# Performance work log

Measured on AMD Instinct MI355X. Metric: run time of the kernel, lower is better.

The kernel has to match this reference:

```python
import jax, jax.numpy as jnp
import numpy as np

MASK_FILL = jnp.float32(-2**32 + 1)

def dice(x, alpha):
    # x: (S, B, F); batch-dim (dim=0) mean/std, unbiased std like torch.std
    avg = x.mean(axis=0)
    std = jnp.std(x, axis=0, ddof=1)
    p = jax.nn.sigmoid((x - avg) / std)
    return x * p + alpha * x * (1.0 - p)

def setup_inputs() -> dict:
    key = jax.random.key(0)
    ks = jax.random.split(key, 12)
    S, B, D = 200, 1024, 128          # seq_len, batch, 2H
    F = 4 * D                          # num_features = 512
    L1, L2 = 80, 40
    inp = {
        "query": jax.random.normal(ks[0], (B, D), jnp.float32),
        "facts": jax.random.normal(ks[1], (S, B, D), jnp.float32),
        "mask": jax.random.randint(ks[2], (S, B), 0, 2).astype(bool),
        "W1": jax.random.normal(ks[3], (F, L1), jnp.float32) / np.sqrt(F),
        "b1": jnp.zeros((L1,), jnp.float32),
        "a1": jnp.zeros((1,), jnp.float32),
        "W2": jax.random.normal(ks[4], (L1, L2), jnp.float32) / np.sqrt(L1),
        "b2": jnp.zeros((L2,), jnp.float32),
        "a2": jnp.zeros((1,), jnp.float32),
        "W3": jax.random.normal(ks[5], (L2, 1), jnp.float32) / np.sqrt(L2),
        "b3": jnp.zeros((1,), jnp.float32),
    }
    return inp

def reference(query, facts, mask, W1, b1, a1, W2, b2, a2, W3, b3):
    S, B, D = facts.shape
    # faithful to torch: tile along feature dim then reshape (permutes elements)
    q2 = jnp.tile(query, (1, S)).reshape(S, B, D)
    x = jnp.concatenate([q2, facts, q2 * facts, q2 - facts], axis=-1)  # (S,B,4D)
    h = dice(jnp.einsum('sbf,fl->sbl', x, W1) + b1, a1)
    h = dice(jnp.einsum('sbf,fl->sbl', h, W2) + b2, a2)
    logits = (jnp.einsum('sbf,fl->sbl', h, W3) + b3).squeeze(-1)  # (S,B)
    masked = jnp.where(mask, logits, MASK_FILL)
    normalized = jax.nn.softmax(masked, axis=0)
    return normalized[..., None] * facts  # (S,B,D)
```

## Files before the change

### kernel.cpp

```cpp
#include <hip/hip_runtime.h>
#include <hip/hip_bf16.h>
#include <math.h>

#define SS 200
#define BB 1024
#define DD 128
#define FF 512
#define LL1 80
#define LL2 40
#define PP (SS*BB)
#define MASK_FILL_F (-4294967295.0f)

typedef short bf16x8 __attribute__((ext_vector_type(8)));
typedef float f32x4  __attribute__((ext_vector_type(4)));

static __device__ __forceinline__ unsigned short f2bf(float x) {
    __hip_bfloat16 h = __float2bfloat16(x);
    return *reinterpret_cast<unsigned short*>(&h);
}
static __device__ __forceinline__ float bf2f(unsigned short u) {
    __hip_bfloat16 h = *reinterpret_cast<__hip_bfloat16*>(&u);
    return __bfloat162float(h);
}
static __device__ __forceinline__ void split8(const float* x, bf16x8& ah, bf16x8& al) {
#pragma unroll
    for (int j = 0; j < 8; ++j) {
        unsigned u = __float_as_uint(x[j]);
        ah[j] = (short)(u >> 16);
        float hi = __uint_as_float(u & 0xffff0000u);
        al[j] = (short)f2bf(x[j] - hi);
    }
}

__global__ void k_prep_all(const float* __restrict__ W1, const float* __restrict__ W2,
                           const unsigned char* __restrict__ mask,
                           unsigned short* __restrict__ bfr1,
                           unsigned short* __restrict__ bfr2, int* __restrict__ flag) {
    const int blk = blockIdx.x;
    if (blk == 35) {
        if (threadIdx.x == 0) {
            int f = 0;
            for (int i = 0; i < 256; ++i)
                if ((i & 3) && mask[i]) f = 1;
            *flag = f;
        }
        return;
    }
    if (blk < 30) {
        int t = blk * 256 + threadIdx.x;
        if (t >= 120 * 64) return;
        int lane = t & 63;
        int fid  = t >> 6;
        int nt   = fid % 5;
        int hl   = (fid / 5) % 2;
        int step = (fid / 10) % 6;
        int h    = fid / 60;
        int ktL  = step / 3;
        int seg  = step - 3 * ktL;
        int kt   = h * 2 + ktL;
        int n     = nt * 16 + (lane & 15);
        int kbase = kt * 32 + (lane >> 4) * 8;
        unsigned short* o = bfr1 + (size_t)t * 8;
#pragma unroll
        for (int j = 0; j < 8; ++j) {
            int k = kbase + j;
            float w;
            if (seg == 0)      w = W1[k * LL1 + n] + W1[(384 + k) * LL1 + n];
            else if (seg == 1) w = W1[(128 + k) * LL1 + n] - W1[(384 + k) * LL1 + n];
            else               w = W1[(256 + k) * LL1 + n];
            unsigned short hb = f2bf(w);
            o[j] = (hl == 0) ? hb : f2bf(w - bf2f(hb));
        }
    } else {
        int t = (blk - 30) * 256 + threadIdx.x;
        if (t >= 18 * 64) return;
        int lane = t & 63;
        int fid  = t >> 6;
        int hl   = fid & 1;
        int nt   = (fid >> 1) % 3;
        int kt   = fid / 6;
        int n  = nt * 16 + (lane & 15);
        int kb = kt * 32 + (lane >> 4) * 8;
        unsigned short* o = bfr2 + (size_t)t * 8;
#pragma unroll
        for (int j = 0; j < 8; ++j) {
            int k = kb + j;
            float w = (k < LL1 && n < LL2) ? W2[k * LL2 + n] : 0.f;
            unsigned short hb = f2bf(w);
            o[j] = (hl == 0) ? hb : f2bf(w - bf2f(hb));
        }
    }
}

__global__ __launch_bounds__(256, 2) void k1_mfma(
    const float* __restrict__ query, const float* __restrict__ facts,
    const unsigned short* __restrict__ bfr, const float* __restrict__ b1,
    float* __restrict__ z1) {
    const int tid  = threadIdx.x;
    const int lane = tid & 63;
    const int m    = lane & 15;
    const int quad = lane >> 4;
    const int pw   = blockIdx.x * 128 + (tid >> 6) * 32;

    __shared__ unsigned short lbuf[30720];

    f32x4 acc[2][5];
#pragma unroll
    for (int t = 0; t < 2; ++t)
#pragma unroll
        for (int nt = 0; nt < 5; ++nt) acc[t][nt] = (f32x4){0.f, 0.f, 0.f, 0.f};

    int pr[2], qr[2];
#pragma unroll
    for (int t = 0; t < 2; ++t) {
        pr[t] = pw + t * 16 + m;
        qr[t] = pr[t] / SS;
    }

    float q8[2][2][8], f8[2][2][8];

#pragma unroll 1
    for (int h = 0; h < 2; ++h) {
#pragma unroll
        for (int ktL = 0; ktL < 2; ++ktL) {
            const int dbase = (h * 2 + ktL) * 32 + quad * 8;
#pragma unroll
            for (int t = 0; t < 2; ++t) {
                *(float4*)&q8[ktL][t][0] = *(const float4*)(query + (size_t)qr[t] * DD + dbase);
                *(float4*)&q8[ktL][t][4] = *(const float4*)(query + (size_t)qr[t] * DD + dbase + 4);
                *(float4*)&f8[ktL][t][0] = *(const float4*)(facts + (size_t)pr[t] * DD + dbase);
                *(float4*)&f8[ktL][t][4] = *(const float4*)(facts + (size_t)pr[t] * DD + dbase + 4);
            }
        }
        if (h) __syncthreads();
        {
            const int4* src = (const int4*)bfr + h * 3840 + tid;
#pragma unroll
            for (int it = 0; it < 15; ++it) {
                int4 v = src[it * 256];
                *(int4*)((char*)lbuf + it * 4096 + tid * 16) = v;
            }
        }
        __syncthreads();

#pragma unroll
        for (int ktL = 0; ktL < 2; ++ktL) {
#pragma unroll
            for (int seg = 0; seg < 3; ++seg) {
                const int step = ktL * 3 + seg;
                bf16x8 Bh[5], Bl[5];
#pragma unroll
                for (int nt = 0; nt < 5; ++nt) {
                    Bh[nt] = *(const bf16x8*)&lbuf[((step * 2 + 0) * 5 + nt) * 512 + lane * 8];
                    Bl[nt] = *(const bf16x8*)&lbuf[((step * 2 + 1) * 5 + nt) * 512 + lane * 8];
                }
#pragma unroll
                for (int t = 0; t < 2; ++t) {
                    float x8[8];
#pragma unroll
                    for (int j = 0; j < 8; ++j)
                        x8[j] = (seg == 0) ? q8[ktL][t][j]
                              : (seg == 1 ? f8[ktL][t][j]
                                          : q8[ktL][t][j] * f8[ktL][t][j]);
                    bf16x8 ah, al;
                    split8(x8, ah, al);
#pragma unroll
                    for (int nt = 0; nt < 5; ++nt) {
                        acc[t][nt] = __builtin_amdgcn_mfma_f32_16x16x32_bf16(ah, Bh[nt], acc[t][nt], 0, 0, 0);
                        acc[t][nt] = __builtin_amdgcn_mfma_f32_16x16x32_bf16(al, Bh[nt], acc[t][nt], 0, 0, 0);
                        acc[t][nt] = __builtin_amdgcn_mfma_f32_16x16x32_bf16(ah, Bl[nt], acc[t][nt], 0, 0, 0);
                    }
                }
            }
        }
    }
#pragma unroll
    for (int t = 0; t < 2; ++t)
#pragma unroll
        for (int nt = 0; nt < 5; ++nt) {
            int n = nt * 16 + m;
            float bias = b1[n];
#pragma unroll
            for (int r = 0; r < 4; ++r)
                z1[(size_t)(pw + t * 16 + quad * 4 + r) * LL1 + n] = acc[t][nt][r] + bias;
        }
}

__global__ __launch_bounds__(256) void k_msd(
    const float* __restrict__ z, float* __restrict__ mean, float* __restrict__ istd) {
    const int col = blockIdx.x * 256 + threadIdx.x;
    const float* p = z + col;
    float s = 0.f, q = 0.f;
#pragma unroll 10
    for (int i = 0; i < SS; ++i) {
        float v = p[(size_t)i * (BB * LL1)];
        s += v;
        q = fmaf(v, v, q);
    }
    float mn = s * (1.f / SS);
    float var = (q - (float)SS * mn * mn) * (1.f / (SS - 1));
    mean[col] = mn;
    istd[col] = rsqrtf(var);
}

__global__ __launch_bounds__(256, 4) void k2_mfma(
    const float* __restrict__ z1, const float* __restrict__ mean1,
    const float* __restrict__ istd1, const float* __restrict__ a1,
    const unsigned short* __restrict__ bfr2, const float* __restrict__ b2,
    float* __restrict__ z2T) {
    const int tid  = threadIdx.x;
    const int lane = tid & 63;
    const int m    = lane & 15;
    const int quad = lane >> 4;
    const int pw   = blockIdx.x * 128 + (tid >> 6) * 32;
    const float alpha = *a1;

    __shared__ unsigned short lb2[9216];
    for (int i = tid; i < 1152; i += 256)
        ((int4*)lb2)[i] = ((const int4*)bfr2)[i];
    __syncthreads();

    f32x4 acc[2][3];
#pragma unroll
    for (int t = 0; t < 2; ++t)
#pragma unroll
        for (int nt = 0; nt < 3; ++nt) acc[t][nt] = (f32x4){0.f, 0.f, 0.f, 0.f};

    float b2v[3];
#pragma unroll
    for (int nt = 0; nt < 3; ++nt) {
        int n = nt * 16 + m;
        b2v[nt] = (n < LL2) ? b2[n] : 0.f;
    }

#pragma unroll
    for (int kt = 0; kt < 3; ++kt) {
        bf16x8 Bh[3], Bl[3];
#pragma unroll
        for (int nt = 0; nt < 3; ++nt) {
            Bh[nt] = *(const bf16x8*)&lb2[((kt * 3 + nt) * 2 + 0) * 512 + lane * 8];
            Bl[nt] = *(const bf16x8*)&lb2[((kt * 3 + nt) * 2 + 1) * 512 + lane * 8];
        }
        const int kb = kt * 32 + quad * 8;
        const bool live = (kt < 2 || quad < 2);
#pragma unroll
        for (int t = 0; t < 2; ++t) {
            const int p = pw + t * 16 + m;
            const int b = p & (BB - 1);
            float x8[8];
            if (live) {
                const float* zr = z1    + (size_t)p * LL1 + kb;
                const float* mu = mean1 + (size_t)b * LL1 + kb;
                const float* is = istd1 + (size_t)b * LL1 + kb;
                float vv[8], mv[8], iv[8];
                *(float4*)&vv[0] = *(const float4*)zr;
                *(float4*)&vv[4] = *(const float4*)(zr + 4);
                *(float4*)&mv[0] = *(const float4*)mu;
                *(float4*)&mv[4] = *(const float4*)(mu + 4);
                *(float4*)&iv[0] = *(const float4*)is;
                *(float4*)&iv[4] = *(const float4*)(is + 4);
#pragma unroll
                for (int j = 0; j < 8; ++j) {
                    float pp = 1.f / (1.f + expf(-(vv[j] - mv[j]) * iv[j]));
                    x8[j] = vv[j] * (alpha + (1.f - alpha) * pp);
                }
            } else {
#pragma unroll
                for (int j = 0; j < 8; ++j) x8[j] = 0.f;
            }
            bf16x8 ah, al;
            split8(x8, ah, al);
#pragma unroll
            for (int nt = 0; nt < 3; ++nt) {
                acc[t][nt] = __builtin_amdgcn_mfma_f32_16x16x32_bf16(ah, Bh[nt], acc[t][nt], 0, 0, 0);
                acc[t][nt] = __builtin_amdgcn_mfma_f32_16x16x32_bf16(al, Bh[nt], acc[t][nt], 0, 0, 0);
                acc[t][nt] = __builtin_amdgcn_mfma_f32_16x16x32_bf16(ah, Bl[nt], acc[t][nt], 0, 0, 0);
            }
        }
    }
#pragma unroll
    for (int t = 0; t < 2; ++t)
#pragma unroll
        for (int r = 0; r < 4; ++r) {
            const int prow = pw + t * 16 + quad * 4 + r;
            const int br = prow & (BB - 1);
            const int sr = prow >> 10;
            float* o = z2T + (size_t)br * (SS * LL2) + (size_t)sr * LL2;
#pragma unroll
            for (int nt = 0; nt < 3; ++nt) {
                int n = nt * 16 + m;
                if (n < LL2) o[n] = acc[t][nt][r] + b2v[nt];
            }
        }
}

__global__ __launch_bounds__(256) void k3_fused(
    const float* __restrict__ z2T, const float* __restrict__ a2,
    const float* __restrict__ W3, const float* __restrict__ b3,
    const void* __restrict__ mask, const int* __restrict__ flag,
    float* __restrict__ wbufT) {
    const int b   = blockIdx.x;
    const int tid = threadIdx.x;
    __shared__ float lds[SS * 41];
    __shared__ float psum[6 * LL2], pssq[6 * LL2];
    __shared__ float smean[LL2], sistd[LL2], sw3[LL2];
    __shared__ float red[4];

    const float4* src = (const float4*)(z2T + (size_t)b * (SS * LL2));
    for (int i = tid; i < (SS * LL2) / 4; i += 256) {
        float4 v = src[i];
        int s = i / 10;
        int o = (i - s * 10) * 4;
        float* d = &lds[s * 41 + o];
        d[0] = v.x; d[1] = v.y; d[2] = v.z; d[3] = v.w;
    }
    __syncthreads();
    if (tid < 240) {
        int l = tid % LL2, c = tid / LL2;
        int s0 = c * 34, s1 = (c == 5) ? SS : s0 + 34;
        float sum = 0.f, ssq = 0.f;
        for (int s = s0; s < s1; ++s) {
            float v = lds[s * 41 + l];
            sum += v;
            ssq = fmaf(v, v, ssq);
        }
        psum[c * LL2 + l] = sum;
        pssq[c * LL2 + l] = ssq;
    }
    __syncthreads();
    if (tid < LL2) {
        float sum = 0.f, ssq = 0.f;
#pragma unroll
        for (int c = 0; c < 6; ++c) {
            sum += psum[c * LL2 + tid];
            ssq += pssq[c * LL2 + tid];
        }
        float mean = sum * (1.f / SS);
        float var  = (ssq - (float)SS * mean * mean) * (1.f / (SS - 1));
        smean[tid] = mean;
        sistd[tid] = rsqrtf(var);
        sw3[tid]   = W3[tid];
    }
    __syncthreads();
    const float alpha = *a2;
    const int boolLayout = *flag;

    float logit = -3.0e38f;
    if (tid < SS) {
        float dot = b3[0];
#pragma unroll
        for (int k = 0; k < LL2; ++k) {
            float v  = lds[tid * 41 + k];
            float pp = 1.f / (1.f + expf(-(v - smean[k]) * sistd[k]));
            float h  = v * (pp + alpha * (1.f - pp));
            dot = fmaf(h, sw3[k], dot);
        }
        int mi = tid * BB + b;
        bool mk = boolLayout ? (((const unsigned char*)mask)[mi] != 0)
                             : (((const int*)mask)[mi] != 0);
        logit = mk ? dot : MASK_FILL_F;
    }
    float v = logit;
#pragma unroll
    for (int off = 1; off < 64; off <<= 1) v = fmaxf(v, __shfl_xor(v, off, 64));
    if ((tid & 63) == 0) red[tid >> 6] = v;
    __syncthreads();
    float smax = fmaxf(fmaxf(red[0], red[1]), fmaxf(red[2], red[3]));
    __syncthreads();
    float e = (tid < SS) ? expf(logit - smax) : 0.f;
    v = e;
#pragma unroll
    for (int off = 1; off < 64; off <<= 1) v += __shfl_xor(v, off, 64);
    if ((tid & 63) == 0) red[tid >> 6] = v;
    __syncthreads();
    float inv = 1.f / (red[0] + red[1] + red[2] + red[3]);
    if (tid < SS) wbufT[(size_t)b * SS + tid] = e * inv;
}

__global__ __launch_bounds__(256) void k4_scale(
    const float* __restrict__ wbufT, const float* __restrict__ facts,
    float* __restrict__ out) {
    int i = blockIdx.x * 256 + threadIdx.x;
    int p = i >> 5;
    float w = wbufT[(size_t)(p & (BB - 1)) * SS + (p >> 10)];
    float4 f = ((const float4*)facts)[i];
    float4 o;
    o.x = f.x * w; o.y = f.y * w; o.z = f.z * w; o.w = f.w * w;
    ((float4*)out)[i] = o;
}

extern "C" void kernel_launch(void* const* d_in, const int* in_sizes, int n_in,
                              void* d_out, int out_size, void* d_ws, size_t ws_size,
                              hipStream_t stream) {
    const float* query = (const float*)d_in[0];
    const float* facts = (const float*)d_in[1];
    const void*  mask  = d_in[2];
    const float* W1 = (const float*)d_in[3];
    const float* b1 = (const float*)d_in[4];
    const float* a1 = (const float*)d_in[5];
    const float* W2 = (const float*)d_in[6];
    const float* b2 = (const float*)d_in[7];
    const float* a2 = (const float*)d_in[8];
    const float* W3 = (const float*)d_in[9];
    const float* b3 = (const float*)d_in[10];
    float* out = (float*)d_out;

    float* z1  = out;
    float* z2T = out + (size_t)PP * LL1;
    float* mean1 = out + 24576000;
    float* istd1 = out + 24657920;
    unsigned short* bfr1 = (unsigned short*)(out + 24739840);
    unsigned short* bfr2 = (unsigned short*)(out + 24801280);
    float* wbufT = (float*)d_ws;
    int*   flag  = (int*)((char*)d_ws + 900 * 1024);

    k_prep_all<<<36, 256, 0, stream>>>(W1, W2, (const unsigned char*)mask, bfr1, bfr2, flag);
    k1_mfma<<<PP / 128, 256, 0, stream>>>(query, facts, bfr1, b1, z1);
    k_msd<<<(BB * LL1) / 256, 256, 0, stream>>>(z1, mean1, istd1);
    k2_mfma<<<PP / 128, 256, 0, stream>>>(z1, mean1, istd1, a1, bfr2, b2, z2T);
    k3_fused<<<BB, 256, 0, stream>>>(z2T, a2, W3, b3, mask, flag, wbufT);
    k4_scale<<<(PP * DD) / (256 * 4), 256, 0, stream>>>(wbufT, facts, out);
}
```

Baseline: 311.6 us.

## Fuse MLP layers, batch-norm stats, softmax and scaling into one per-batch kernel

```diff
diff --git a/kernel.cpp b/kernel.cpp
--- a/kernel.cpp
+++ b/kernel.cpp
@@ -10,6 +10,7 @@
 #define LL2 40
 #define PP (SS*BB)
 #define MASK_FILL_F (-4294967295.0f)
+#define NTILE 13
 
 typedef short bf16x8 __attribute__((ext_vector_type(8)));
 typedef float f32x4  __attribute__((ext_vector_type(4)));
@@ -92,177 +93,174 @@
     }
 }
 
-__global__ __launch_bounds__(256, 2) void k1_mfma(
+__global__ __launch_bounds__(256, 2) void k_fused(
     const float* __restrict__ query, const float* __restrict__ facts,
-    const unsigned short* __restrict__ bfr, const float* __restrict__ b1,
-    float* __restrict__ z1) {
+    const unsigned short* __restrict__ bfr1, const unsigned short* __restrict__ bfr2,
+    const float* __restrict__ b1, const float* __restrict__ a1,
+    const float* __restrict__ b2, const float* __restrict__ a2,
+    const float* __restrict__ W3, const float* __restrict__ b3,
+    const void* __restrict__ mask, const int* __restrict__ flag,
+    float* __restrict__ out) {
     const int tid  = threadIdx.x;
+    const int w    = tid >> 6;
     const int lane = tid & 63;
     const int m    = lane & 15;
     const int quad = lane >> 4;
-    const int pw   = blockIdx.x * 128 + (tid >> 6) * 32;
-
-    __shared__ unsigned short lbuf[30720];
-
-    f32x4 acc[2][5];
-#pragma unroll
-    for (int t = 0; t < 2; ++t)
+    const int b    = blockIdx.x;
+
+    __shared__ __align__(16) float z1f[NTILE * 16 * 81 + 16];
+    __shared__ float psum[240], pssq[240];
+    __shared__ float smean[LL1], sistd[LL1];
+    __shared__ float sw3[LL2];
+    __shared__ float red[4];
+    __shared__ float wgt[SS];
+
+    int tile[4], pr[4], qr[4];
+    bool tl[4];
+#pragma unroll
+    for (int t = 0; t < 4; ++t) {
+        tile[t] = t * 4 + w;
+        tl[t]   = (tile[t] < NTILE);
+        int s = tile[t] * 16 + m;
+        if (s > SS - 1) s = SS - 1;
+        pr[t] = s * BB + b;
+        qr[t] = pr[t] / SS;
+    }
+
+    f32x4 acc[4][5];
+#pragma unroll
+    for (int t = 0; t < 4; ++t)
 #pragma unroll
         for (int nt = 0; nt < 5; ++nt) acc[t][nt] = (f32x4){0.f, 0.f, 0.f, 0.f};
-
-    int pr[2], qr[2];
-#pragma unroll
-    for (int t = 0; t < 2; ++t) {
-        pr[t] = pw + t * 16 + m;
-        qr[t] = pr[t] / SS;
-    }
-
-    float q8[2][2][8], f8[2][2][8];
 
 #pragma unroll 1
     for (int h = 0; h < 2; ++h) {
+        if (h) __syncthreads();
+        {
+            const int4* src = (const int4*)bfr1 + h * 3840 + tid;
+            int4* dst = (int4*)z1f;
+#pragma unroll
+            for (int it = 0; it < 15; ++it)
+                dst[it * 256 + tid] = src[it * 256];
+        }
+        __syncthreads();
+        const unsigned short* lbuf = (const unsigned short*)z1f;
 #pragma unroll
         for (int ktL = 0; ktL < 2; ++ktL) {
             const int dbase = (h * 2 + ktL) * 32 + quad * 8;
 #pragma unroll
-            for (int t = 0; t < 2; ++t) {
-                *(float4*)&q8[ktL][t][0] = *(const float4*)(query + (size_t)qr[t] * DD + dbase);
-                *(float4*)&q8[ktL][t][4] = *(const float4*)(query + (size_t)qr[t] * DD + dbase + 4);
-                *(float4*)&f8[ktL][t][0] = *(const float4*)(facts + (size_t)pr[t] * DD + dbase);
-                *(float4*)&f8[ktL][t][4] = *(const float4*)(facts + (size_t)pr[t] * DD + dbase + 4);
-            }
-        }
-        if (h) __syncthreads();
-        {
-            const int4* src = (const int4*)bfr + h * 3840 + tid;
-#pragma unroll
-            for (int it = 0; it < 15; ++it) {
-                int4 v = src[it * 256];
-                *(int4*)((char*)lbuf + it * 4096 + tid * 16) = v;
-            }
-        }
-        __syncthreads();
-
-#pragma unroll
-        for (int ktL = 0; ktL < 2; ++ktL) {
-#pragma unroll
-            for (int seg = 0; seg < 3; ++seg) {
-                const int step = ktL * 3 + seg;
-                bf16x8 Bh[5], Bl[5];
-#pragma unroll
-                for (int nt = 0; nt < 5; ++nt) {
-                    Bh[nt] = *(const bf16x8*)&lbuf[((step * 2 + 0) * 5 + nt) * 512 + lane * 8];
-                    Bl[nt] = *(const bf16x8*)&lbuf[((step * 2 + 1) * 5 + nt) * 512 + lane * 8];
+            for (int tp = 0; tp < 2; ++tp) {
+                float q8[2][8], f8[2][8];
+#pragma unroll
+                for (int u = 0; u < 2; ++u) {
+                    const int t = tp * 2 + u;
+                    const float* qp = query + (size_t)qr[t] * DD + dbase;
+                    const float* fp = facts + (size_t)pr[t] * DD + dbase;
+                    *(float4*)&q8[u][0] = *(const float4*)qp;
+                    *(float4*)&q8[u][4] = *(const float4*)(qp + 4);
+                    *(float4*)&f8[u][0] = *(const float4*)fp;
+                    *(float4*)&f8[u][4] = *(const float4*)(fp + 4);
                 }
 #pragma unroll
-                for (int t = 0; t < 2; ++t) {
-                    float x8[8];
-#pragma unroll
-                    for (int j = 0; j < 8; ++j)
-                        x8[j] = (seg == 0) ? q8[ktL][t][j]
-                              : (seg == 1 ? f8[ktL][t][j]
-                                          : q8[ktL][t][j] * f8[ktL][t][j]);
-                    bf16x8 ah, al;
-                    split8(x8, ah, al);
+                for (int seg = 0; seg < 3; ++seg) {
+                    const int step = ktL * 3 + seg;
+                    bf16x8 Bh[5], Bl[5];
 #pragma unroll
                     for (int nt = 0; nt < 5; ++nt) {
-                        acc[t][nt] = __builtin_amdgcn_mfma_f32_16x16x32_bf16(ah, Bh[nt], acc[t][nt], 0, 0, 0);
-                        acc[t][nt] = __builtin_amdgcn_mfma_f32_16x16x32_bf16(al, Bh[nt], acc[t][nt], 0, 0, 0);
-                        acc[t][nt] = __builtin_amdgcn_mfma_f32_16x16x32_bf16(ah, Bl[nt], acc[t][nt], 0, 0, 0);
+                        Bh[nt] = *(const bf16x8*)&lbuf[((step * 2 + 0) * 5 + nt) * 512 + lane * 8];
+                        Bl[nt] = *(const bf16x8*)&lbuf[((step * 2 + 1) * 5 + nt) * 512 + lane * 8];
+                    }
+#pragma unroll
+                    for (int u = 0; u < 2; ++u) {
+                        const int t = tp * 2 + u;
+                        if (!tl[t]) continue;
+                        float x8[8];
+#pragma unroll
+                        for (int j = 0; j < 8; ++j)
+                            x8[j] = (seg == 0) ? q8[u][j]
+                                  : (seg == 1 ? f8[u][j] : q8[u][j] * f8[u][j]);
+                        bf16x8 ah, al;
+                        split8(x8, ah, al);
+#pragma unroll
+                        for (int nt = 0; nt < 5; ++nt) {
+                            acc[t][nt] = __builtin_amdgcn_mfma_f32_16x16x32_bf16(ah, Bh[nt], acc[t][nt], 0, 0, 0);
+                            acc[t][nt] = __builtin_amdgcn_mfma_f32_16x16x32_bf16(al, Bh[nt], acc[t][nt], 0, 0, 0);
+                            acc[t][nt] = __builtin_amdgcn_mfma_f32_16x16x32_bf16(ah, Bl[nt], acc[t][nt], 0, 0, 0);
+                        }
                     }
                 }
             }
         }
     }
-#pragma unroll
-    for (int t = 0; t < 2; ++t)
-#pragma unroll
-        for (int nt = 0; nt < 5; ++nt) {
-            int n = nt * 16 + m;
-            float bias = b1[n];
-#pragma unroll
-            for (int r = 0; r < 4; ++r)
-                z1[(size_t)(pw + t * 16 + quad * 4 + r) * LL1 + n] = acc[t][nt][r] + bias;
-        }
-}
-
-__global__ __launch_bounds__(256) void k_msd(
-    const float* __restrict__ z, float* __restrict__ mean, float* __restrict__ istd) {
-    const int col = blockIdx.x * 256 + threadIdx.x;
-    const float* p = z + col;
-    float s = 0.f, q = 0.f;
-#pragma unroll 10
-    for (int i = 0; i < SS; ++i) {
-        float v = p[(size_t)i * (BB * LL1)];
-        s += v;
-        q = fmaf(v, v, q);
-    }
-    float mn = s * (1.f / SS);
-    float var = (q - (float)SS * mn * mn) * (1.f / (SS - 1));
-    mean[col] = mn;
-    istd[col] = rsqrtf(var);
-}
-
-__global__ __launch_bounds__(256, 4) void k2_mfma(
-    const float* __restrict__ z1, const float* __restrict__ mean1,
-    const float* __restrict__ istd1, const float* __restrict__ a1,
-    const unsigned short* __restrict__ bfr2, const float* __restrict__ b2,
-    float* __restrict__ z2T) {
-    const int tid  = threadIdx.x;
-    const int lane = tid & 63;
-    const int m    = lane & 15;
-    const int quad = lane >> 4;
-    const int pw   = blockIdx.x * 128 + (tid >> 6) * 32;
-    const float alpha = *a1;
-
-    __shared__ unsigned short lb2[9216];
-    for (int i = tid; i < 1152; i += 256)
-        ((int4*)lb2)[i] = ((const int4*)bfr2)[i];
-    __syncthreads();
-
-    f32x4 acc[2][3];
-#pragma unroll
-    for (int t = 0; t < 2; ++t)
-#pragma unroll
-        for (int nt = 0; nt < 3; ++nt) acc[t][nt] = (f32x4){0.f, 0.f, 0.f, 0.f};
-
-    float b2v[3];
-#pragma unroll
-    for (int nt = 0; nt < 3; ++nt) {
-        int n = nt * 16 + m;
-        b2v[nt] = (n < LL2) ? b2[n] : 0.f;
-    }
+
+    __syncthreads();
+    {
+        float b1v[5];
+#pragma unroll
+        for (int nt = 0; nt < 5; ++nt) b1v[nt] = b1[nt * 16 + m];
+#pragma unroll
+        for (int t = 0; t < 4; ++t) {
+            if (!tl[t]) continue;
+#pragma unroll
+            for (int nt = 0; nt < 5; ++nt)
+#pragma unroll
+                for (int r = 0; r < 4; ++r)
+                    z1f[(tile[t] * 16 + quad * 4 + r) * 81 + nt * 16 + m] = acc[t][nt][r] + b1v[nt];
+        }
+    }
+    __syncthreads();
+
+    if (tid < 240) {
+        const int l = tid % LL1, c = tid / LL1;
+        const int s0 = c * 67, s1 = (c == 2) ? SS : s0 + 67;
+        float sum = 0.f, ssq = 0.f;
+        for (int s = s0; s < s1; ++s) {
+            float v = z1f[s * 81 + l];
+            sum += v;
+            ssq = fmaf(v, v, ssq);
+        }
+        psum[c * LL1 + l] = sum;
+        pssq[c * LL1 + l] = ssq;
+    }
+    __syncthreads();
+    if (tid < LL1) {
+        float sum = psum[tid] + psum[LL1 + tid] + psum[2 * LL1 + tid];
+        float ssq = pssq[tid] + pssq[LL1 + tid] + pssq[2 * LL1 + tid];
+        float mn  = sum * (1.f / SS);
+        float var = (ssq - (float)SS * mn * mn) * (1.f / (SS - 1));
+        smean[tid] = mn;
+        sistd[tid] = rsqrtf(var);
+    }
+    __syncthreads();
+
+    const float alpha1 = *a1;
+    f32x4 acc2[4][3];
+#pragma unroll
+    for (int t = 0; t < 4; ++t)
+#pragma unroll
+        for (int nt = 0; nt < 3; ++nt) acc2[t][nt] = (f32x4){0.f, 0.f, 0.f, 0.f};
 
 #pragma unroll
     for (int kt = 0; kt < 3; ++kt) {
         bf16x8 Bh[3], Bl[3];
 #pragma unroll
         for (int nt = 0; nt < 3; ++nt) {
-            Bh[nt] = *(const bf16x8*)&lb2[((kt * 3 + nt) * 2 + 0) * 512 + lane * 8];
-            Bl[nt] = *(const bf16x8*)&lb2[((kt * 3 + nt) * 2 + 1) * 512 + lane * 8];
+            Bh[nt] = *(const bf16x8*)(bfr2 + (size_t)((kt * 3 + nt) * 2 + 0) * 512 + lane * 8);
+            Bl[nt] = *(const bf16x8*)(bfr2 + (size_t)((kt * 3 + nt) * 2 + 1) * 512 + lane * 8);
         }
         const int kb = kt * 32 + quad * 8;
-        const bool live = (kt < 2 || quad < 2);
-#pragma unroll
-        for (int t = 0; t < 2; ++t) {
-            const int p = pw + t * 16 + m;
-            const int b = p & (BB - 1);
+        const bool lv = (kt < 2 || quad < 2);
+#pragma unroll
+        for (int t = 0; t < 4; ++t) {
+            if (!tl[t]) continue;
             float x8[8];
-            if (live) {
-                const float* zr = z1    + (size_t)p * LL1 + kb;
-                const float* mu = mean1 + (size_t)b * LL1 + kb;
-                const float* is = istd1 + (size_t)b * LL1 + kb;
-                float vv[8], mv[8], iv[8];
-                *(float4*)&vv[0] = *(const float4*)zr;
-                *(float4*)&vv[4] = *(const float4*)(zr + 4);
-                *(float4*)&mv[0] = *(const float4*)mu;
-                *(float4*)&mv[4] = *(const float4*)(mu + 4);
-                *(float4*)&iv[0] = *(const float4*)is;
-                *(float4*)&iv[4] = *(const float4*)(is + 4);
+            if (lv) {
+                const float* zr = &z1f[(tile[t] * 16 + m) * 81 + kb];
 #pragma unroll
                 for (int j = 0; j < 8; ++j) {
-                    float pp = 1.f / (1.f + expf(-(vv[j] - mv[j]) * iv[j]));
-                    x8[j] = vv[j] * (alpha + (1.f - alpha) * pp);
+                    float v  = zr[j];
+                    float pp = 1.f / (1.f + expf(-(v - smean[kb + j]) * sistd[kb + j]));
+                    x8[j] = v * (alpha1 + (1.f - alpha1) * pp);
                 }
             } else {
 #pragma unroll
@@ -272,55 +270,44 @@
             split8(x8, ah, al);
 #pragma unroll
             for (int nt = 0; nt < 3; ++nt) {
-                acc[t][nt] = __builtin_amdgcn_mfma_f32_16x16x32_bf16(ah, Bh[nt], acc[t][nt], 0, 0, 0);
-                acc[t][nt] = __builtin_amdgcn_mfma_f32_16x16x32_bf16(al, Bh[nt], acc[t][nt], 0, 0, 0);
-                acc[t][nt] = __builtin_amdgcn_mfma_f32_16x16x32_bf16(ah, Bl[nt], acc[t][nt], 0, 0, 0);
+                acc2[t][nt] = __builtin_amdgcn_mfma_f32_16x16x32_bf16(ah, Bh[nt], acc2[t][nt], 0, 0, 0);
+                acc2[t][nt] = __builtin_amdgcn_mfma_f32_16x16x32_bf16(al, Bh[nt], acc2[t][nt], 0, 0, 0);
+                acc2[t][nt] = __builtin_amdgcn_mfma_f32_16x16x32_bf16(ah, Bl[nt], acc2[t][nt], 0, 0, 0);
             }
         }
     }
-#pragma unroll
-    for (int t = 0; t < 2; ++t)
-#pragma unroll
-        for (int r = 0; r < 4; ++r) {
-            const int prow = pw + t * 16 + quad * 4 + r;
-            const int br = prow & (BB - 1);
-            const int sr = prow >> 10;
-            float* o = z2T + (size_t)br * (SS * LL2) + (size_t)sr * LL2;
-#pragma unroll
-            for (int nt = 0; nt < 3; ++nt) {
-                int n = nt * 16 + m;
-                if (n < LL2) o[n] = acc[t][nt][r] + b2v[nt];
+    __syncthreads();
+
+    {
+        float b2v[3];
+#pragma unroll
+        for (int nt = 0; nt < 3; ++nt) {
+            const int n = nt * 16 + m;
+            b2v[nt] = (n < LL2) ? b2[n] : 0.f;
+        }
+#pragma unroll
+        for (int t = 0; t < 4; ++t) {
+            if (!tl[t]) continue;
+#pragma unroll
+            for (int r = 0; r < 4; ++r) {
+                const int srow = tile[t] * 16 + quad * 4 + r;
+                if (srow >= SS) continue;
+#pragma unroll
+                for (int nt = 0; nt < 3; ++nt) {
+                    const int n = nt * 16 + m;
+                    if (n < LL2) z1f[srow * 41 + n] = acc2[t][nt][r] + b2v[nt];
+                }
             }
         }
-}
-
-__global__ __launch_bounds__(256) void k3_fused(
-    const float* __restrict__ z2T, const float* __restrict__ a2,
-    const float* __restrict__ W3, const float* __restrict__ b3,
-    const void* __restrict__ mask, const int* __restrict__ flag,
-    float* __restrict__ wbufT) {
-    const int b   = blockIdx.x;
-    const int tid = threadIdx.x;
-    __shared__ float lds[SS * 41];
-    __shared__ float psum[6 * LL2], pssq[6 * LL2];
-    __shared__ float smean[LL2], sistd[LL2], sw3[LL2];
-    __shared__ float red[4];
-
-    const float4* src = (const float4*)(z2T + (size_t)b * (SS * LL2));
-    for (int i = tid; i < (SS * LL2) / 4; i += 256) {
-        float4 v = src[i];
-        int s = i / 10;
-        int o = (i - s * 10) * 4;
-        float* d = &lds[s * 41 + o];
-        d[0] = v.x; d[1] = v.y; d[2] = v.z; d[3] = v.w;
-    }
-    __syncthreads();
+    }
+    __syncthreads();
+
     if (tid < 240) {
-        int l = tid % LL2, c = tid / LL2;
-        int s0 = c * 34, s1 = (c == 5) ? SS : s0 + 34;
+        const int l = tid % LL2, c = tid / LL2;
+        const int s0 = c * 34, s1 = (c == 5) ? SS : s0 + 34;
         float sum = 0.f, ssq = 0.f;
         for (int s = s0; s < s1; ++s) {
-            float v = lds[s * 41 + l];
+            float v = z1f[s * 41 + l];
             sum += v;
             ssq = fmaf(v, v, ssq);
         }
@@ -335,29 +322,29 @@
             sum += psum[c * LL2 + tid];
             ssq += pssq[c * LL2 + tid];
         }
-        float mean = sum * (1.f / SS);
-        float var  = (ssq - (float)SS * mean * mean) * (1.f / (SS - 1));
-        smean[tid] = mean;
+        float mn  = sum * (1.f / SS);
+        float var = (ssq - (float)SS * mn * mn) * (1.f / (SS - 1));
+        smean[tid] = mn;
         sistd[tid] = rsqrtf(var);
         sw3[tid]   = W3[tid];
     }
     __syncthreads();
-    const float alpha = *a2;
+
+    const float alpha2 = *a2;
     const int boolLayout = *flag;
-
     float logit = -3.0e38f;
     if (tid < SS) {
         float dot = b3[0];
 #pragma unroll
         for (int k = 0; k < LL2; ++k) {
-            float v  = lds[tid * 41 + k];
+            float v  = z1f[tid * 41 + k];
             float pp = 1.f / (1.f + expf(-(v - smean[k]) * sistd[k]));
-            float h  = v * (pp + alpha * (1.f - pp));
-            dot = fmaf(h, sw3[k], dot);
-        }
-        int mi = tid * BB + b;
-        bool mk = boolLayout ? (((const unsigned char*)mask)[mi] != 0)
-                             : (((const int*)mask)[mi] != 0);
+            float hh = v * (pp + alpha2 * (1.f - pp));
+            dot = fmaf(hh, sw3[k], dot);
+        }
+        const int mi = tid * BB + b;
+        const bool mk = boolLayout ? (((const unsigned char*)mask)[mi] != 0)
+                                   : (((const int*)mask)[mi] != 0);
         logit = mk ? dot : MASK_FILL_F;
     }
     float v = logit;
@@ -365,28 +352,31 @@
     for (int off = 1; off < 64; off <<= 1) v = fmaxf(v, __shfl_xor(v, off, 64));
     if ((tid & 63) == 0) red[tid >> 6] = v;
     __syncthreads();
-    float smax = fmaxf(fmaxf(red[0], red[1]), fmaxf(red[2], red[3]));
-    __syncthreads();
-    float e = (tid < SS) ? expf(logit - smax) : 0.f;
+    const float smax = fmaxf(fmaxf(red[0], red[1]), fmaxf(red[2], red[3]));
+    __syncthreads();
+    const float e = (tid < SS) ? expf(logit - smax) : 0.f;
     v = e;
 #pragma unroll
     for (int off = 1; off < 64; off <<= 1) v += __shfl_xor(v, off, 64);
     if ((tid & 63) == 0) red[tid >> 6] = v;
     __syncthreads();
-    float inv = 1.f / (red[0] + red[1] + red[2] + red[3]);
-    if (tid < SS) wbufT[(size_t)b * SS + tid] = e * inv;
-}
-
-__global__ __launch_bounds__(256) void k4_scale(
-    const float* __restrict__ wbufT, const float* __restrict__ facts,
-    float* __restrict__ out) {
-    int i = blockIdx.x * 256 + threadIdx.x;
-    int p = i >> 5;
-    float w = wbufT[(size_t)(p & (BB - 1)) * SS + (p >> 10)];
-    float4 f = ((const float4*)facts)[i];
-    float4 o;
-    o.x = f.x * w; o.y = f.y * w; o.z = f.z * w; o.w = f.w * w;
-    ((float4*)out)[i] = o;
+    const float inv = 1.f / (red[0] + red[1] + red[2] + red[3]);
+    if (tid < SS) wgt[tid] = e * inv;
+    __syncthreads();
+
+    const float4* f4 = (const float4*)facts;
+    float4* o4 = (float4*)out;
+#pragma unroll 5
+    for (int i = tid; i < SS * 32; i += 256) {
+        const int s  = i >> 5;
+        const int d4 = i & 31;
+        const size_t idx = (size_t)(s * BB + b) * 32 + d4;
+        float4 f = f4[idx];
+        const float ww = wgt[s];
+        float4 o;
+        o.x = f.x * ww; o.y = f.y * ww; o.z = f.z * ww; o.w = f.w * ww;
+        o4[idx] = o;
+    }
 }
 
 extern "C" void kernel_launch(void* const* d_in, const int* in_sizes, int n_in,
@@ -403,21 +393,12 @@
     const float* a2 = (const float*)d_in[8];
     const float* W3 = (const float*)d_in[9];
     const float* b3 = (const float*)d_in[10];
-    float* out = (float*)d_out;
-
-    float* z1  = out;
-    float* z2T = out + (size_t)PP * LL1;
-    float* mean1 = out + 24576000;
-    float* istd1 = out + 24657920;
-    unsigned short* bfr1 = (unsigned short*)(out + 24739840);
-    unsigned short* bfr2 = (unsigned short*)(out + 24801280);
-    float* wbufT = (float*)d_ws;
-    int*   flag  = (int*)((char*)d_ws + 900 * 1024);
+
+    unsigned short* bfr1 = (unsigned short*)d_ws;
+    unsigned short* bfr2 = (unsigned short*)((char*)d_ws + 131072);
+    int* flag = (int*)((char*)d_ws + 163840);
 
     k_prep_all<<<36, 256, 0, stream>>>(W1, W2, (const unsigned char*)mask, bfr1, bfr2, flag);
-    k1_mfma<<<PP / 128, 256, 0, stream>>>(query, facts, bfr1, b1, z1);
-    k_msd<<<(BB * LL1) / 256, 256, 0, stream>>>(z1, mean1, istd1);
-    k2_mfma<<<PP / 128, 256, 0, stream>>>(z1, mean1, istd1, a1, bfr2, b2, z2T);
-    k3_fused<<<BB, 256, 0, stream>>>(z2T, a2, W3, b3, mask, flag, wbufT);
-    k4_scale<<<(PP * DD) / (256 * 4), 256, 0, stream>>>(wbufT, facts, out);
-}
+    k_fused<<<BB, 256, 0, stream>>>(query, facts, bfr1, bfr2, b1, a1, b2, a2,
+                                    W3, b3, mask, flag, (float*)d_out);
+}
```

Result: slower. 319.7 us (+2.6%).
